# Kernel optimization log

Hardware: AMD Instinct MI355X
Metric: run time of the kernel (lower is better)

The kernel has to match this reference:

```python
import jax, jax.numpy as jnp
import numpy as np

N = 100000
E = 3200000
D = 128
EPS = 1e-5


def setup_inputs() -> dict:
    key = jax.random.key(0)
    ks = jax.random.split(key, 9)
    h = jax.random.normal(ks[0], (N, D), dtype=jnp.float32)
    src = jax.random.randint(ks[1], (E,), 0, N, dtype=jnp.int64)
    dst = jax.random.randint(ks[2], (E,), 0, N, dtype=jnp.int64)
    s = 1.0 / np.sqrt(D)
    W_self = jax.random.uniform(ks[3], (D, D), jnp.float32, -s, s)
    W_neigh = jax.random.uniform(ks[4], (D, D), jnp.float32, -s, s)
    b = jax.random.uniform(ks[5], (D,), jnp.float32, -s, s)
    gamma = jnp.ones((D,), jnp.float32)
    beta = jnp.zeros((D,), jnp.float32)
    return {"h": h, "src": src, "dst": dst, "W_self": W_self,
            "W_neigh": W_neigh, "b": b, "gamma": gamma, "beta": beta}


def reference(h, src, dst, W_self, W_neigh, b, gamma, beta):
    # --- SAGEConv, mean aggregator (dropout p=0 -> identity) ---
    # gather source features along edges, segment-mean into destination nodes
    neigh_sum = jax.ops.segment_sum(h[src], dst, num_segments=N)      # [N, D]
    deg = jax.ops.segment_sum(jnp.ones((E,), h.dtype), dst, num_segments=N)
    neigh = neigh_sum / jnp.maximum(deg, 1.0)[:, None]                # [N, D]
    rst = h @ W_self + neigh @ W_neigh + b                            # [N, D]
    rst = jax.nn.relu(rst)                                            # activation
    # --- BatchNorm1d (training-mode batch statistics) ---
    mean = jnp.mean(rst, axis=0)
    var = jnp.var(rst, axis=0)
    rst = (rst - mean) * jax.lax.rsqrt(var + EPS) * gamma + beta
    # --- residual (in_feats == out_feats) ---
    return h + rst
```

## Files before the change

### kernel.cpp

```cpp
#include <hip/hip_runtime.h>

#define DCAP 2432
#define NBMAX 1600
#define GB 1024

typedef __attribute__((ext_vector_type(2))) float f32x2;
typedef __attribute__((ext_vector_type(4))) float f32x4;
typedef __attribute__((ext_vector_type(8))) short bf16x8;

__device__ __forceinline__ unsigned short f2bf(float f) {
  union { float f; unsigned u; } c; c.f = f;
  unsigned u = c.u;
  unsigned r = u + 0x7FFFu + ((u >> 16) & 1u);
  return (unsigned short)(r >> 16);
}
__device__ __forceinline__ float bf2f(unsigned short s) {
  union { unsigned u; float f; } c; c.u = ((unsigned)s) << 16;
  return c.f;
}

__global__ void k_convert(const float* __restrict__ h, unsigned short* __restrict__ X,
                          unsigned* __restrict__ X8, int nnodes) {
  int stride = gridDim.x * blockDim.x;
  int total = nnodes * 32;
  for (int i = blockIdx.x * blockDim.x + threadIdx.x; i < total; i += stride) {
    int n = i >> 5, c = i & 31;
    float4 v = *(const float4*)(h + (long)n * 128 + c * 4);
    ushort4 o;
    o.x = f2bf(v.x); o.y = f2bf(v.y); o.z = f2bf(v.z); o.w = f2bf(v.w);
    *(ushort4*)(X + (long)n * 256 + c * 4) = o;
    int p8 = __builtin_amdgcn_cvt_pk_fp8_f32(v.x, v.y, 0, false);
    p8 = __builtin_amdgcn_cvt_pk_fp8_f32(v.z, v.w, p8, true);
    X8[(long)n * 32 + c] = (unsigned)p8;
  }
}

__global__ __launch_bounds__(512) void k_part(const int* __restrict__ dst,
                                              const int* __restrict__ src,
                                              int* __restrict__ gcur,
                                              unsigned* __restrict__ buck,
                                              int E, int NB) {
  __shared__ int cnt[NBMAX];
  __shared__ int cur[NBMAX];
  int t = threadIdx.x;
  int chunk = (E + gridDim.x - 1) / gridDim.x;
  int e0 = blockIdx.x * chunk;
  int e1 = e0 + chunk; if (e1 > E) e1 = E;
  for (int i = t; i < NB; i += 512) cnt[i] = 0;
  __syncthreads();
  for (int e = e0 + t; e < e1; e += 512)
    atomicAdd(&cnt[dst[e] >> 6], 1);
  __syncthreads();
  for (int i = t; i < NB; i += 512) {
    int c = cnt[i];
    cur[i] = c ? atomicAdd(&gcur[i], c) : 0;
  }
  __syncthreads();
  for (int e = e0 + t; e < e1; e += 512) {
    int d = dst[e];
    int b = d >> 6;
    int p = atomicAdd(&cur[b], 1);
    if (p < DCAP)
      buck[(long)b * DCAP + p] = ((unsigned)src[e] << 6) | (unsigned)(d & 63);
  }
}

__global__ void k_wprep(const float* __restrict__ Ws, const float* __restrict__ Wn,
                        unsigned short* __restrict__ Wt) {
  int i = blockIdx.x * blockDim.x + threadIdx.x;
  if (i >= 128 * 256) return;
  int col = i >> 8, k = i & 255;
  float v = (k < 128) ? Ws[k * 128 + col] : Wn[(k - 128) * 128 + col];
  Wt[col * 256 + k] = f2bf(v);
}

__global__ __launch_bounds__(256) void k_aggb(unsigned short* __restrict__ X,
                                              const unsigned* __restrict__ X8,
                                              const unsigned* __restrict__ buck,
                                              const int* __restrict__ gcur,
                                              int nnodes) {
  __shared__ unsigned eload[DCAP];
  __shared__ unsigned eord[DCAP];
  __shared__ int dcnt[64], dstart[64], dcur[64], sc[64];
  int t = threadIdx.x;
  int b = blockIdx.x;
  int cntE = gcur[b]; if (cntE > DCAP) cntE = DCAP;
  if (t < 64) dcnt[t] = 0;
  __syncthreads();
  for (int i = t; i < cntE; i += 256) {
    unsigned p = buck[(long)b * DCAP + i];
    eload[i] = p;
    atomicAdd(&dcnt[p & 63u], 1);
  }
  __syncthreads();
  if (t < 64) sc[t] = dcnt[t];
  __syncthreads();
  for (int off = 1; off < 64; off <<= 1) {
    int v = (t < 64 && t >= off) ? sc[t - off] : 0;
    __syncthreads();
    if (t < 64) sc[t] += v;
    __syncthreads();
  }
  if (t < 64) { int ex = sc[t] - dcnt[t]; dstart[t] = ex; dcur[t] = ex; }
  __syncthreads();
  for (int i = t; i < cntE; i += 256) {
    unsigned p = eload[i];
    int pos = atomicAdd(&dcur[p & 63u], 1);
    eord[pos] = p >> 6;
  }
  __syncthreads();

  int lane = t & 63, w = t >> 6;
  int half = lane >> 5, hl = lane & 31;
  int ndst = nnodes - b * 64; if (ndst > 64) ndst = 64;
  for (int dl = w; dl < ndst; dl += 4) {
    int n = b * 64 + dl;
    int start = dstart[dl], dn = dcnt[dl];
    f32x2 a01[2], a23[2];
#pragma unroll
    for (int u = 0; u < 2; u++) {
      a01[u].x = 0.f; a01[u].y = 0.f;
      a23[u].x = 0.f; a23[u].y = 0.f;
    }
    int i = 0;
    for (; i + 16 <= dn; i += 16) {
      unsigned v[8];
#pragma unroll
      for (int u = 0; u < 8; u++) {
        int e = (int)eord[start + i + 2 * u + half];
        v[u] = X8[(long)e * 32 + hl];
      }
#pragma unroll
      for (int u = 0; u < 8; u++) {
        a01[u & 1] += __builtin_amdgcn_cvt_pk_f32_fp8(v[u], false);
        a23[u & 1] += __builtin_amdgcn_cvt_pk_f32_fp8(v[u], true);
      }
    }
    for (; i + 2 <= dn; i += 2) {
      int e = (int)eord[start + i + half];
      unsigned v = X8[(long)e * 32 + hl];
      a01[0] += __builtin_amdgcn_cvt_pk_f32_fp8(v, false);
      a23[0] += __builtin_amdgcn_cvt_pk_f32_fp8(v, true);
    }
    if (i < dn && half == 0) {
      int e = (int)eord[start + i];
      unsigned v = X8[(long)e * 32 + hl];
      a01[0] += __builtin_amdgcn_cvt_pk_f32_fp8(v, false);
      a23[0] += __builtin_amdgcn_cvt_pk_f32_fp8(v, true);
    }
    float s0 = a01[0].x + a01[1].x;
    float s1 = a01[0].y + a01[1].y;
    float s2 = a23[0].x + a23[1].x;
    float s3 = a23[0].y + a23[1].y;
    s0 += __shfl_down(s0, 32);
    s1 += __shfl_down(s1, 32);
    s2 += __shfl_down(s2, 32);
    s3 += __shfl_down(s3, 32);
    if (half == 0) {
      float scl = 1.0f / fmaxf((float)dn, 1.0f);
      ushort4 o;
      o.x = f2bf(s0 * scl); o.y = f2bf(s1 * scl);
      o.z = f2bf(s2 * scl); o.w = f2bf(s3 * scl);
      *(ushort4*)(X + (long)n * 256 + 128 + hl * 4) = o;
    }
  }
}

__global__ __launch_bounds__(256) void k_gemm(const unsigned short* __restrict__ X,
                                              const unsigned short* __restrict__ Wt,
                                              const float* __restrict__ bias,
                                              unsigned short* __restrict__ rst8,
                                              float* __restrict__ psum,
                                              float* __restrict__ psq,
                                              int nnodes, int ntiles) {
  int t = threadIdx.x;
  int w = t >> 6, lane = t & 63;
  int m = lane & 15, q = lane >> 4;
  int col0 = w * 32 + m;
  int col1 = col0 + 16;
  bf16x8 b0[8], b1[8];
#pragma unroll
  for (int ks = 0; ks < 8; ks++) {
    b0[ks] = *(const bf16x8*)(Wt + col0 * 256 + q * 8 + ks * 32);
    b1[ks] = *(const bf16x8*)(Wt + col1 * 256 + q * 8 + ks * 32);
  }
  float bv0 = bias[col0], bv1 = bias[col1];
  float s0 = 0.f, sq0 = 0.f, s1 = 0.f, sq1 = 0.f;

  for (int tb = blockIdx.x; tb < ntiles; tb += GB) {
    int rowm = tb * 16 + m; if (rowm >= nnodes) rowm = nnodes - 1;
    const unsigned short* xp = X + (long)rowm * 256 + q * 8;
    bf16x8 a[8];
#pragma unroll
    for (int ks = 0; ks < 8; ks++) a[ks] = *(const bf16x8*)(xp + ks * 32);
    f32x4 acc0 = {0.f, 0.f, 0.f, 0.f};
    f32x4 acc1 = {0.f, 0.f, 0.f, 0.f};
#pragma unroll
    for (int ks = 0; ks < 8; ks++) {
      acc0 = __builtin_amdgcn_mfma_f32_16x16x32_bf16(a[ks], b0[ks], acc0, 0, 0, 0);
      acc1 = __builtin_amdgcn_mfma_f32_16x16x32_bf16(a[ks], b1[ks], acc1, 0, 0, 0);
    }
#pragma unroll
    for (int r = 0; r < 4; r++) {
      int row = tb * 16 + q * 4 + r;
      if (row < nnodes) {
        float v0 = acc0[r] + bv0; v0 = v0 > 0.f ? v0 : 0.f;
        float v1 = acc1[r] + bv1; v1 = v1 > 0.f ? v1 : 0.f;
        rst8[(long)row * 128 + col0] = f2bf(v0);
        rst8[(long)row * 128 + col1] = f2bf(v1);
        s0 += v0; sq0 += v0 * v0;
        s1 += v1; sq1 += v1 * v1;
      }
    }
  }
  s0 += __shfl_down(s0, 32);  s0 += __shfl_down(s0, 16);
  sq0 += __shfl_down(sq0, 32); sq0 += __shfl_down(sq0, 16);
  s1 += __shfl_down(s1, 32);  s1 += __shfl_down(s1, 16);
  sq1 += __shfl_down(sq1, 32); sq1 += __shfl_down(sq1, 16);
  if (lane < 16) {
    long o = (long)blockIdx.x * 128;
    psum[o + col0] = s0;  psum[o + col1] = s1;
    psq[o + col0] = sq0;  psq[o + col1] = sq1;
  }
}

__global__ __launch_bounds__(1024) void k_redstat(const float* __restrict__ psum,
                                                  const float* __restrict__ psq,
                                                  const float* __restrict__ gamma,
                                                  const float* __restrict__ beta,
                                                  float* __restrict__ scale,
                                                  float* __restrict__ shift, float Nf) {
  __shared__ float l1[1024], l2[1024];
  int t = threadIdx.x;
  int col = t & 127, sl = t >> 7;
  float s = 0.f, s2 = 0.f;
  for (int b = sl; b < GB; b += 8) {
    s += psum[b * 128 + col];
    s2 += psq[b * 128 + col];
  }
  l1[t] = s; l2[t] = s2;
  __syncthreads();
  if (t < 128) {
#pragma unroll
    for (int i = 1; i < 8; i++) { s += l1[t + i * 128]; s2 += l2[t + i * 128]; }
    float mean = s / Nf;
    float var = s2 / Nf - mean * mean;
    float inv = rsqrtf(var + 1e-5f);
    float scv = gamma[t] * inv;
    scale[t] = scv;
    shift[t] = beta[t] - mean * scv;
  }
}

__global__ void k_final(const float* __restrict__ h, float* __restrict__ out,
                        const unsigned short* __restrict__ rst8,
                        const float* __restrict__ scale, const float* __restrict__ shift,
                        int nnodes) {
  __shared__ float sc_s[128], sh_s[128];
  int t = threadIdx.x;
  if (t < 128) { sc_s[t] = scale[t]; sh_s[t] = shift[t]; }
  __syncthreads();
  int stride = gridDim.x * blockDim.x;
  int total = nnodes * 16;
  for (int i = blockIdx.x * blockDim.x + threadIdx.x; i < total; i += stride) {
    int c = i & 15;
    uint4 rv = *(const uint4*)(rst8 + (long)i * 8);
    float4 h0 = *(const float4*)(h + (long)i * 8);
    float4 h1 = *(const float4*)(h + (long)i * 8 + 4);
    float4 sc0 = *(const float4*)(sc_s + c * 8);
    float4 sc1 = *(const float4*)(sc_s + c * 8 + 4);
    float4 sh0 = *(const float4*)(sh_s + c * 8);
    float4 sh1 = *(const float4*)(sh_s + c * 8 + 4);
    float4 o0, o1;
    o0.x = h0.x + bf2f((unsigned short)(rv.x & 0xFFFFu)) * sc0.x + sh0.x;
    o0.y = h0.y + bf2f((unsigned short)(rv.x >> 16)) * sc0.y + sh0.y;
    o0.z = h0.z + bf2f((unsigned short)(rv.y & 0xFFFFu)) * sc0.z + sh0.z;
    o0.w = h0.w + bf2f((unsigned short)(rv.y >> 16)) * sc0.w + sh0.w;
    o1.x = h1.x + bf2f((unsigned short)(rv.z & 0xFFFFu)) * sc1.x + sh1.x;
    o1.y = h1.y + bf2f((unsigned short)(rv.z >> 16)) * sc1.y + sh1.y;
    o1.z = h1.z + bf2f((unsigned short)(rv.w & 0xFFFFu)) * sc1.z + sh1.z;
    o1.w = h1.w + bf2f((unsigned short)(rv.w >> 16)) * sc1.w + sh1.w;
    *(float4*)(out + (long)i * 8) = o0;
    *(float4*)(out + (long)i * 8 + 4) = o1;
  }
}

extern "C" void kernel_launch(void* const* d_in, const int* in_sizes, int n_in,
                              void* d_out, int out_size, void* d_ws, size_t ws_size,
                              hipStream_t stream) {
  const float* h     = (const float*)d_in[0];
  const int*   src   = (const int*)d_in[1];
  const int*   dst   = (const int*)d_in[2];
  const float* Ws    = (const float*)d_in[3];
  const float* Wn    = (const float*)d_in[4];
  const float* bias  = (const float*)d_in[5];
  const float* gamma = (const float*)d_in[6];
  const float* beta  = (const float*)d_in[7];
  float* out = (float*)d_out;

  int nnodes = in_sizes[0] / 128;
  int E = in_sizes[1];
  int NB = (nnodes + 63) >> 6;
  int ntiles = (nnodes + 15) >> 4;

  char* ws = (char*)d_ws;
  size_t off = 0;
  unsigned short* X = (unsigned short*)(ws + off); off += (size_t)nnodes * 256 * 2;
  size_t off_alias = off;
  unsigned* X8 = (unsigned*)(ws + off);            off += (size_t)nnodes * 128;
  unsigned* buck = (unsigned*)(ws + off);          off += (size_t)NB * DCAP * 4;
  unsigned short* rst8 = (unsigned short*)(ws + off_alias);
  size_t zoff = off;
  int* gcur = (int*)(ws + off);                    off += NBMAX * 4;
  unsigned short* Wt = (unsigned short*)(ws + off); off += 128 * 256 * 2;
  float* psum = (float*)(ws + off);                off += (size_t)GB * 128 * 4;
  float* psq = (float*)(ws + off);                 off += (size_t)GB * 128 * 4;
  float* scale = (float*)(ws + off);               off += 512;
  float* shift = (float*)(ws + off);               off += 512;

  hipMemsetAsync(ws + zoff, 0, NBMAX * 4, stream);

  k_convert<<<4096, 256, 0, stream>>>(h, X, X8, nnodes);
  k_part<<<256, 512, 0, stream>>>(dst, src, gcur, buck, E, NB);
  k_wprep<<<128, 256, 0, stream>>>(Ws, Wn, Wt);
  k_aggb<<<NB, 256, 0, stream>>>(X, X8, buck, gcur, nnodes);
  k_gemm<<<GB, 256, 0, stream>>>(X, Wt, bias, rst8, psum, psq, nnodes, ntiles);
  k_redstat<<<1, 1024, 0, stream>>>(psum, psq, gamma, beta, scale, shift, (float)nnodes);
  k_final<<<4096, 256, 0, stream>>>(h, out, rst8, scale, shift, nnodes);
}
```

Before: 354.2 us.

## Split edge partitioning into count, prefix-scan offsets, and scatter kernels

Replaces the single-pass bucket partition, which reserved slots through global atomics on per-bucket cursors, with three kernels. A count kernel writes per-block bucket histograms, a scan kernel computes exclusive per-block offsets and bucket totals, and a scatter kernel places edges using those offsets. This removes the global atomics and the memset, and makes bucket placement deterministic per block. In exchange the dst array is read twice, two extra kernel launches are added, and the count matrices are written and read.

```diff
diff --git a/kernel.cpp b/kernel.cpp
--- a/kernel.cpp
+++ b/kernel.cpp
@@ -2,6 +2,7 @@
 
 #define DCAP 2432
 #define NBMAX 1600
+#define PB 256
 #define GB 1024
 
 typedef __attribute__((ext_vector_type(2))) float f32x2;
@@ -35,28 +36,53 @@
   }
 }
 
-__global__ __launch_bounds__(512) void k_part(const int* __restrict__ dst,
-                                              const int* __restrict__ src,
-                                              int* __restrict__ gcur,
-                                              unsigned* __restrict__ buck,
-                                              int E, int NB) {
+__global__ __launch_bounds__(1024) void k_cnt(const int* __restrict__ dst,
+                                              int* __restrict__ cnt_mat, int E, int NB) {
   __shared__ int cnt[NBMAX];
-  __shared__ int cur[NBMAX];
   int t = threadIdx.x;
   int chunk = (E + gridDim.x - 1) / gridDim.x;
   int e0 = blockIdx.x * chunk;
   int e1 = e0 + chunk; if (e1 > E) e1 = E;
-  for (int i = t; i < NB; i += 512) cnt[i] = 0;
-  __syncthreads();
-  for (int e = e0 + t; e < e1; e += 512)
+  for (int i = t; i < NB; i += 1024) cnt[i] = 0;
+  __syncthreads();
+  for (int e = e0 + t; e < e1; e += 1024)
     atomicAdd(&cnt[dst[e] >> 6], 1);
   __syncthreads();
-  for (int i = t; i < NB; i += 512) {
-    int c = cnt[i];
-    cur[i] = c ? atomicAdd(&gcur[i], c) : 0;
-  }
-  __syncthreads();
-  for (int e = e0 + t; e < e1; e += 512) {
+  for (int i = t; i < NB; i += 1024)
+    cnt_mat[blockIdx.x * NBMAX + i] = cnt[i];
+}
+
+__global__ __launch_bounds__(PB) void k_ofs(const int* __restrict__ cnt_mat,
+                                            int* __restrict__ ofs_mat,
+                                            int* __restrict__ gcur, int NB) {
+  __shared__ int l[PB];
+  int b = blockIdx.x, t = threadIdx.x;
+  int v = cnt_mat[t * NBMAX + b];
+  l[t] = v;
+  __syncthreads();
+  for (int off = 1; off < PB; off <<= 1) {
+    int add = (t >= off) ? l[t - off] : 0;
+    __syncthreads();
+    l[t] += add;
+    __syncthreads();
+  }
+  int ex = l[t] - v;
+  ofs_mat[t * NBMAX + b] = ex;
+  if (t == PB - 1) gcur[b] = l[t];
+}
+
+__global__ __launch_bounds__(1024) void k_scat(const int* __restrict__ dst,
+                                               const int* __restrict__ src,
+                                               const int* __restrict__ ofs_mat,
+                                               unsigned* __restrict__ buck, int E, int NB) {
+  __shared__ int cur[NBMAX];
+  int t = threadIdx.x;
+  int chunk = (E + gridDim.x - 1) / gridDim.x;
+  int e0 = blockIdx.x * chunk;
+  int e1 = e0 + chunk; if (e1 > E) e1 = E;
+  for (int i = t; i < NB; i += 1024) cur[i] = ofs_mat[blockIdx.x * NBMAX + i];
+  __syncthreads();
+  for (int e = e0 + t; e < e1; e += 1024) {
     int d = dst[e];
     int b = d >> 6;
     int p = atomicAdd(&cur[b], 1);
@@ -310,18 +336,19 @@
   unsigned* X8 = (unsigned*)(ws + off);            off += (size_t)nnodes * 128;
   unsigned* buck = (unsigned*)(ws + off);          off += (size_t)NB * DCAP * 4;
   unsigned short* rst8 = (unsigned short*)(ws + off_alias);
-  size_t zoff = off;
   int* gcur = (int*)(ws + off);                    off += NBMAX * 4;
   unsigned short* Wt = (unsigned short*)(ws + off); off += 128 * 256 * 2;
   float* psum = (float*)(ws + off);                off += (size_t)GB * 128 * 4;
   float* psq = (float*)(ws + off);                 off += (size_t)GB * 128 * 4;
   float* scale = (float*)(ws + off);               off += 512;
   float* shift = (float*)(ws + off);               off += 512;
-
-  hipMemsetAsync(ws + zoff, 0, NBMAX * 4, stream);
+  int* cnt_mat = (int*)(ws + off);                 off += (size_t)PB * NBMAX * 4;
+  int* ofs_mat = (int*)(ws + off);                 off += (size_t)PB * NBMAX * 4;
 
   k_convert<<<4096, 256, 0, stream>>>(h, X, X8, nnodes);
-  k_part<<<256, 512, 0, stream>>>(dst, src, gcur, buck, E, NB);
+  k_cnt<<<PB, 1024, 0, stream>>>(dst, cnt_mat, E, NB);
+  k_ofs<<<NB, PB, 0, stream>>>(cnt_mat, ofs_mat, gcur, NB);
+  k_scat<<<PB, 1024, 0, stream>>>(dst, src, ofs_mat, buck, E, NB);
   k_wprep<<<128, 256, 0, stream>>>(Ws, Wn, Wt);
   k_aggb<<<NB, 256, 0, stream>>>(X, X8, buck, gcur, nnodes);
   k_gemm<<<GB, 256, 0, stream>>>(X, Wt, bias, rst8, psum, psq, nnodes, ntiles);
```

Result: no change. 356.5 us (+0.6%).
